# Kernel tuning notes

Hardware: AMD Instinct MI355X
Metric: run time of the kernel (lower is better)

Reference implementation:

```python
import jax, jax.numpy as jnp
import numpy as np

N = 50000      # nodes
E = 500000     # edges
IN = 128       # input feature dim
HID = 64       # hidden per-head dim
CLS = 64       # num classes
SLOPE = 0.2    # leaky_relu negative slope


def _gat_layer(x, W, al, ar, src, dst):
    """One GATConv: project, per-edge score, edge-softmax over dst, weighted aggregate.
    x: [N, Din], W: [Din, H*F], al/ar: [H, F]. Returns [N, H, F]."""
    H, F = al.shape
    n = x.shape[0]
    feat = (x @ W).reshape(n, H, F)                      # [N,H,F]
    el = jnp.einsum('nhf,hf->nh', feat, al)              # [N,H]
    er = jnp.einsum('nhf,hf->nh', feat, ar)              # [N,H]
    e = el[src] + er[dst]                                # u_add_v -> [E,H]
    e = jnp.where(e >= 0, e, SLOPE * e)                  # leaky_relu
    # edge_softmax over destination nodes (numerically stable)
    m = jax.lax.stop_gradient(jax.ops.segment_max(e, dst, num_segments=n))
    ex = jnp.exp(e - m[dst])
    denom = jax.ops.segment_sum(ex, dst, num_segments=n)
    a = ex / denom[dst]                                  # [E,H]
    # u_mul_e + sum aggregation
    out = jax.ops.segment_sum(feat[src] * a[:, :, None], dst, num_segments=n)
    return out                                           # [N,H,F]


def setup_inputs() -> dict:
    key = jax.random.key(0)
    ks = jax.random.split(key, 12)
    s = 0.05  # xavier-ish scale
    x = jax.random.normal(ks[0], (N, IN), jnp.float32)
    src = jax.random.randint(ks[1], (E,), 0, N)
    dst = jax.random.randint(ks[2], (E,), 0, N)
    W1 = jax.random.normal(ks[3], (IN, 4 * HID), jnp.float32) * s
    al1 = jax.random.normal(ks[4], (4, HID), jnp.float32) * s
    ar1 = jax.random.normal(ks[5], (4, HID), jnp.float32) * s
    W2 = jax.random.normal(ks[6], (4 * HID, 4 * HID), jnp.float32) * s
    al2 = jax.random.normal(ks[7], (4, HID), jnp.float32) * s
    ar2 = jax.random.normal(ks[8], (4, HID), jnp.float32) * s
    W3 = jax.random.normal(ks[9], (4 * HID, CLS), jnp.float32) * s
    al3 = jax.random.normal(ks[10], (1, CLS), jnp.float32) * s
    ar3 = jax.random.normal(ks[11], (1, CLS), jnp.float32) * s
    res_W3 = jax.random.normal(jax.random.fold_in(key, 99), (4 * HID, CLS), jnp.float32) * s
    return {"x": x, "W1": W1, "al1": al1, "ar1": ar1, "W2": W2, "al2": al2,
            "ar2": ar2, "W3": W3, "al3": al3, "ar3": ar3, "res_W3": res_W3,
            "src": src, "dst": dst}


def reference(x, W1, al1, ar1, W2, al2, ar2, W3, al3, ar3, res_W3, src, dst):
    # layer 0: no residual, elu activation, flatten heads
    h = _gat_layer(x, W1, al1, ar1, src, dst)            # [N,4,64]
    h = jax.nn.elu(h).reshape(N, -1)                     # [N,256]
    # layer 1: residual is Identity (in_dst 256 == 4*64), elu, flatten
    h1 = _gat_layer(h, W2, al2, ar2, src, dst)           # [N,4,64]
    h1 = h1 + h.reshape(N, 4, HID)                       # residual (Identity)
    h = jax.nn.elu(h1).reshape(N, -1)                    # [N,256]
    # layer 2: residual Linear 256->64, no activation, mean over heads
    h2 = _gat_layer(h, W3, al3, ar3, src, dst)           # [N,1,64]
    h2 = h2 + (h @ res_W3).reshape(N, 1, CLS)            # residual fc
    logits = h2.mean(axis=1)                             # [N,64]
    return logits
```

## Files before the change

### kernel.cpp

```cpp
#include <hip/hip_runtime.h>
#include <hip/hip_bf16.h>
#include <math.h>

#define SLOPE 0.2f

typedef __attribute__((ext_vector_type(8))) short short8;
typedef __attribute__((ext_vector_type(4))) float f32x4;
typedef __attribute__((ext_vector_type(4))) int   i32x4;

static __device__ __forceinline__ float leakyf(float x) { return x >= 0.f ? x : SLOPE * x; }
static __device__ __forceinline__ float bflo(unsigned u) { return __builtin_bit_cast(float, u << 16); }
static __device__ __forceinline__ float bfhi(unsigned u) { return __builtin_bit_cast(float, u & 0xffff0000u); }
static __device__ __forceinline__ unsigned short f2bf(float f) {
    unsigned u = __builtin_bit_cast(unsigned, f);
    return (unsigned short)((u + 0x7fff + ((u >> 16) & 1)) >> 16);
}

struct __align__(8) us4 { unsigned short a, b, c, d; };


__global__ __launch_bounds__(256) void tconv_all(const float* __restrict__ W1,
                                                 const float* __restrict__ W2,
                                                 const float* __restrict__ W3,
                                                 const float* __restrict__ rW3,
                                                 unsigned short* __restrict__ W1t,
                                                 unsigned short* __restrict__ W2t,
                                                 unsigned short* __restrict__ W3c) {
    int i = blockIdx.x * 256 + threadIdx.x;
    const float* W; unsigned short* Wt; int K, lNc, idx; bool permK;
    if (i < 32768)       { W = W1;  Wt = W1t;            K = 128; lNc = 8; idx = i;          permK = false; }
    else if (i < 98304)  { W = W2;  Wt = W2t;            K = 256; lNc = 8; idx = i - 32768;  permK = true; }
    else if (i < 114688) { W = W3;  Wt = W3c;            K = 256; lNc = 6; idx = i - 98304;  permK = true; }
    else                 { W = rW3; Wt = W3c + 64 * 256; K = 256; lNc = 6; idx = i - 114688; permK = true; }
    int k = idx >> lNc, n = idx & ((1 << lNc) - 1);
    int kp = permK ? ((k & ~63) | (((k & 15) << 2) | ((k & 63) >> 4))) : k;
    Wt[n * K + kp] = f2bf(W[idx]);
}

template<bool A_F32>
__global__ __launch_bounds__(256) void gemm_l12(const void* __restrict__ Av,
                                                const unsigned short* __restrict__ Wt,
                                                unsigned short* __restrict__ outb,
                                                const float* __restrict__ al,
                                                const float* __restrict__ ar,
                                                float* __restrict__ el,
                                                float* __restrict__ er,
                                                int M, int K) {
    const int lane = threadIdx.x & 63;
    const int wid = threadIdx.x >> 6;
    const int rlo = lane & 15;
    const int q = lane >> 4;
    const int kg = q * 8;
    const int m0 = blockIdx.x * 64;
    const int cbase = wid * 64;

    f32x4 acc[4][4];
#pragma unroll
    for (int mf = 0; mf < 4; ++mf)
#pragma unroll
        for (int nf = 0; nf < 4; ++nf) acc[mf][nf] = (f32x4){0.f, 0.f, 0.f, 0.f};

    for (int k0 = 0; k0 < K; k0 += 32) {
        short8 a[4];
#pragma unroll
        for (int mf = 0; mf < 4; ++mf) {
            int r = m0 + mf * 16 + rlo;
            if (r >= M) r = M - 1;
            if (A_F32) {
                const float* ap = (const float*)Av + (size_t)r * K + k0 + kg;
                float4 f0 = *(const float4*)ap;
                float4 f1 = *(const float4*)(ap + 4);
                short8 t;
                t[0] = f2bf(f0.x); t[1] = f2bf(f0.y); t[2] = f2bf(f0.z); t[3] = f2bf(f0.w);
                t[4] = f2bf(f1.x); t[5] = f2bf(f1.y); t[6] = f2bf(f1.z); t[7] = f2bf(f1.w);
                a[mf] = t;
            } else {
                a[mf] = *(const short8*)((const unsigned short*)Av + (size_t)r * K + k0 + kg);
            }
        }
#pragma unroll
        for (int nf = 0; nf < 4; ++nf) {
            short8 b = *(const short8*)(Wt + (size_t)(cbase + nf * 16 + rlo) * K + k0 + kg);
#pragma unroll
            for (int mf = 0; mf < 4; ++mf)
                acc[mf][nf] = __builtin_amdgcn_mfma_f32_16x16x32_bf16(a[mf], b, acc[mf][nf], 0, 0, 0);
        }
    }

    float alv[4], arv[4];
#pragma unroll
    for (int nf = 0; nf < 4; ++nf) {
        alv[nf] = al[cbase + nf * 16 + rlo];
        arv[nf] = ar[cbase + nf * 16 + rlo];
    }

#pragma unroll
    for (int mf = 0; mf < 4; ++mf) {
#pragma unroll
        for (int reg = 0; reg < 4; ++reg) {
            int r = m0 + mf * 16 + q * 4 + reg;
            float pl = 0.f, pr = 0.f;
#pragma unroll
            for (int nf = 0; nf < 4; ++nf) {
                pl += acc[mf][nf][reg] * alv[nf];
                pr += acc[mf][nf][reg] * arv[nf];
            }
#pragma unroll
            for (int off = 1; off < 16; off <<= 1) {
                pl += __shfl_xor(pl, off);
                pr += __shfl_xor(pr, off);
            }
            if (rlo == 0 && r < M) {
                el[(size_t)r * 4 + wid] = pl;
                er[(size_t)r * 4 + wid] = pr;
            }
            if (r < M) {
                us4 o = {f2bf(acc[mf][0][reg]), f2bf(acc[mf][1][reg]),
                         f2bf(acc[mf][2][reg]), f2bf(acc[mf][3][reg])};
                *(us4*)(outb + (size_t)r * 256 + cbase + rlo * 4) = o;
            }
        }
    }
}

__global__ __launch_bounds__(256) void gemm_l3(const unsigned short* __restrict__ A,
                                               const unsigned short* __restrict__ Wt,
                                               unsigned short* __restrict__ featb,
                                               float* __restrict__ resf,
                                               const float* __restrict__ al,
                                               const float* __restrict__ ar,
                                               float* __restrict__ el,
                                               float* __restrict__ er, int M) {
    const int K = 256;
    const int lane = threadIdx.x & 63;
    const int wid = threadIdx.x >> 6;
    const int rlo = lane & 15;
    const int q = lane >> 4;
    const int kg = q * 8;
    const int m0 = blockIdx.x * 128 + (wid >> 1) * 64;
    const int ch = wid & 1;
    const int cbase = ch * 64;

    f32x4 acc[4][4];
#pragma unroll
    for (int mf = 0; mf < 4; ++mf)
#pragma unroll
        for (int nf = 0; nf < 4; ++nf) acc[mf][nf] = (f32x4){0.f, 0.f, 0.f, 0.f};

    for (int k0 = 0; k0 < K; k0 += 32) {
        short8 a[4];
#pragma unroll
        for (int mf = 0; mf < 4; ++mf) {
            int r = m0 + mf * 16 + rlo;
            if (r >= M) r = M - 1;
            a[mf] = *(const short8*)(A + (size_t)r * K + k0 + kg);
        }
#pragma unroll
        for (int nf = 0; nf < 4; ++nf) {
            short8 b = *(const short8*)(Wt + (size_t)(cbase + nf * 16 + rlo) * K + k0 + kg);
#pragma unroll
            for (int mf = 0; mf < 4; ++mf)
                acc[mf][nf] = __builtin_amdgcn_mfma_f32_16x16x32_bf16(a[mf], b, acc[mf][nf], 0, 0, 0);
        }
    }

    float alv[4], arv[4];
    if (ch == 0) {
#pragma unroll
        for (int nf = 0; nf < 4; ++nf) {
            alv[nf] = al[nf * 16 + rlo];
            arv[nf] = ar[nf * 16 + rlo];
        }
    }

#pragma unroll
    for (int mf = 0; mf < 4; ++mf) {
#pragma unroll
        for (int reg = 0; reg < 4; ++reg) {
            int r = m0 + mf * 16 + q * 4 + reg;
            if (ch == 0) {
                float pl = 0.f, pr = 0.f;
#pragma unroll
                for (int nf = 0; nf < 4; ++nf) {
                    pl += acc[mf][nf][reg] * alv[nf];
                    pr += acc[mf][nf][reg] * arv[nf];
                }
#pragma unroll
                for (int off = 1; off < 16; off <<= 1) {
                    pl += __shfl_xor(pl, off);
                    pr += __shfl_xor(pr, off);
                }
                if (rlo == 0 && r < M) { el[r] = pl; er[r] = pr; }
                if (r < M) {
                    us4 o = {f2bf(acc[mf][0][reg]), f2bf(acc[mf][1][reg]),
                             f2bf(acc[mf][2][reg]), f2bf(acc[mf][3][reg])};
                    *(us4*)(featb + (size_t)r * 64 + rlo * 4) = o;
                }
            } else if (r < M) {
                float4 o = {acc[mf][0][reg], acc[mf][1][reg], acc[mf][2][reg], acc[mf][3][reg]};
                *(float4*)(resf + (size_t)r * 64 + rlo * 4) = o;
            }
        }
    }
}

__global__ void hist_kernel(const int* __restrict__ dst, int* __restrict__ counts, int e) {
    int i = blockIdx.x * blockDim.x + threadIdx.x;
    if (i < e) atomicAdd(&counts[dst[i]], 1);
}

__global__ __launch_bounds__(1024) void scan_block(const int* __restrict__ counts,
                                                   int* __restrict__ offsets,
                                                   int* __restrict__ bsums, int n) {
    __shared__ int ws[16];
    int tid = threadIdx.x, lane = tid & 63, wid = tid >> 6;
    int idx = blockIdx.x * 1024 + tid;
    int v = (idx < n) ? counts[idx] : 0;
    int s = v;
#pragma unroll
    for (int off = 1; off < 64; off <<= 1) {
        int t = __shfl_up(s, off);
        if (lane >= off) s += t;
    }
    if (lane == 63) ws[wid] = s;
    __syncthreads();
    if (tid < 16) {
        int w2 = ws[tid];
#pragma unroll
        for (int off = 1; off < 16; off <<= 1) {
            int t = __shfl_up(w2, off);
            if (tid >= off) w2 += t;
        }
        ws[tid] = w2;
    }
    __syncthreads();
    int wpre = wid ? ws[wid - 1] : 0;
    if (idx < n) offsets[idx] = wpre + s - v;
    if (tid == 0) bsums[blockIdx.x] = ws[15];
}

__global__ __launch_bounds__(1024) void add_off(const int* __restrict__ bsums,
                                                int* __restrict__ offsets,
                                                int* __restrict__ cursor, int n, int e, int nb) {
    __shared__ int base_s;
    int tid = threadIdx.x;
    if (tid < 64) {
        int v = (tid < blockIdx.x && tid < nb) ? bsums[tid] : 0;
#pragma unroll
        for (int off = 32; off > 0; off >>= 1) v += __shfl_xor(v, off);
        if (tid == 0) base_s = v;
    }
    __syncthreads();
    int idx = blockIdx.x * 1024 + tid;
    if (idx < n) {
        int v = offsets[idx] + base_s;
        offsets[idx] = v;
        cursor[idx] = v;
    }
    if (idx == 0) offsets[n] = e;
}

__global__ void scatter_kernel(const int* __restrict__ src, const int* __restrict__ dst,
                               int* __restrict__ cursor, int* __restrict__ csr_src,
                               int* __restrict__ csr_dst, int e) {
    int i = blockIdx.x * blockDim.x + threadIdx.x;
    if (i < e) {
        int d = dst[i];
        int pos = atomicAdd(&cursor[d], 1);
        csr_src[pos] = src[i];
        csr_dst[pos] = d;
    }
}

template<int H>
__global__ __launch_bounds__(256) void edge_scores(const int* __restrict__ csr_src,
                                                   const int* __restrict__ csr_dst,
                                                   const float* __restrict__ el,
                                                   const float* __restrict__ er,
                                                   float* __restrict__ w, int E) {
    int e4 = (blockIdx.x * 256 + threadIdx.x) * 4;
    if (e4 >= E) return;
    i32x4 s = *(const i32x4*)(csr_src + e4);
    i32x4 d = *(const i32x4*)(csr_dst + e4);
    if (H == 4) {
        float4 o0, o1, o2, o3;
        float* op[4] = {&o0.x, &o1.x, &o2.x, &o3.x};
#pragma unroll
        for (int j = 0; j < 4; ++j) {
            float4 l = *(const float4*)(el + (size_t)s[j] * 4);
            float4 r = *(const float4*)(er + (size_t)d[j] * 4);
            op[0][j] = __expf(fminf(leakyf(l.x + r.x), 80.f));
            op[1][j] = __expf(fminf(leakyf(l.y + r.y), 80.f));
            op[2][j] = __expf(fminf(leakyf(l.z + r.z), 80.f));
            op[3][j] = __expf(fminf(leakyf(l.w + r.w), 80.f));
        }
        *(float4*)(w + 0 * (size_t)E + e4) = o0;
        *(float4*)(w + 1 * (size_t)E + e4) = o1;
        *(float4*)(w + 2 * (size_t)E + e4) = o2;
        *(float4*)(w + 3 * (size_t)E + e4) = o3;
    } else {
        float4 o;
#pragma unroll
        for (int j = 0; j < 4; ++j)
            (&o.x)[j] = __expf(fminf(leakyf(el[s[j]] + er[d[j]]), 80.f));
        *(float4*)(w + e4) = o;
    }
}

template<int RES, int ACT>
__global__ __launch_bounds__(256) void gat_agg4(const unsigned short* __restrict__ fp,
                                                const float* __restrict__ wbuf,
                                                const int* __restrict__ offsets,
                                                const int* __restrict__ csr_src,
                                                const unsigned short* __restrict__ resid,
                                                unsigned short* __restrict__ outb,
                                                int n, int E) {
    int wv = threadIdx.x >> 6;
    int lane = threadIdx.x & 63;
    int half = lane >> 5;
    int sub = lane & 31;
    int node = blockIdx.x * 8 + wv * 2 + half;

    int e0 = 0, e1 = 0;
    if (node < n) { e0 = offsets[node]; e1 = offsets[node + 1]; }
    int cnt = e1 - e0;
    int ocnt = __shfl_xor(cnt, 32);
    int mc = cnt > ocnt ? cnt : ocnt;

    const float* wb = wbuf + (size_t)(sub >> 3) * E;

    float den = 0.f;
    float acc[8] = {0.f, 0.f, 0.f, 0.f, 0.f, 0.f, 0.f, 0.f};

    for (int t = 0; t < mc; t += 8) {
        i32x4 sv0, sv1;
        f32x4 wv0, wv1;
        __builtin_memcpy(&sv0, csr_src + e0 + t, 16);
        __builtin_memcpy(&sv1, csr_src + e0 + t + 4, 16);
        __builtin_memcpy(&wv0, wb + e0 + t, 16);
        __builtin_memcpy(&wv1, wb + e0 + t + 4, 16);
        int s[8];
        float w[8];
#pragma unroll
        for (int j = 0; j < 8; ++j) {
            bool ok = (t + j) < cnt;
            int sj = (j < 4) ? sv0[j] : sv1[j - 4];
            float wj = (j < 4) ? wv0[j] : wv1[j - 4];
            s[j] = ok ? sj : 0;
            w[j] = ok ? wj : 0.f;
        }
        uint4 u[8];
#pragma unroll
        for (int j = 0; j < 8; ++j)
            u[j] = *(const uint4*)(fp + (size_t)s[j] * 256 + sub * 8);
#pragma unroll
        for (int j = 0; j < 8; ++j) {
            den += w[j];
            acc[0] += w[j] * bflo(u[j].x);
            acc[1] += w[j] * bfhi(u[j].x);
            acc[2] += w[j] * bflo(u[j].y);
            acc[3] += w[j] * bfhi(u[j].y);
            acc[4] += w[j] * bflo(u[j].z);
            acc[5] += w[j] * bfhi(u[j].z);
            acc[6] += w[j] * bflo(u[j].w);
            acc[7] += w[j] * bfhi(u[j].w);
        }
    }

    if (node >= n) return;

    float inv = den > 0.f ? 1.f / den : 0.f;
    float v[8];
#pragma unroll
    for (int i = 0; i < 8; ++i) v[i] = acc[i] * inv;

    if (RES == 1) {
        uint4 ru = *(const uint4*)(resid + (size_t)node * 256 + sub * 8);
        v[0] += bflo(ru.x); v[1] += bfhi(ru.x);
        v[2] += bflo(ru.y); v[3] += bfhi(ru.y);
        v[4] += bflo(ru.z); v[5] += bfhi(ru.z);
        v[6] += bflo(ru.w); v[7] += bfhi(ru.w);
    }
    if (ACT == 1) {
#pragma unroll
        for (int i = 0; i < 8; ++i) v[i] = v[i] > 0.f ? v[i] : __expf(v[i]) - 1.f;
    }
    uint4 o;
    o.x = (unsigned)f2bf(v[0]) | ((unsigned)f2bf(v[1]) << 16);
    o.y = (unsigned)f2bf(v[2]) | ((unsigned)f2bf(v[3]) << 16);
    o.z = (unsigned)f2bf(v[4]) | ((unsigned)f2bf(v[5]) << 16);
    o.w = (unsigned)f2bf(v[6]) | ((unsigned)f2bf(v[7]) << 16);
    *(uint4*)(outb + (size_t)node * 256 + sub * 8) = o;
}

__global__ __launch_bounds__(256) void gat_agg1(const unsigned short* __restrict__ fp,
                                                const float* __restrict__ wbuf,
                                                const int* __restrict__ offsets,
                                                const int* __restrict__ csr_src,
                                                const float* __restrict__ resf,
                                                float* __restrict__ outv, int n, int E) {
    int wv = threadIdx.x >> 6;
    int lane = threadIdx.x & 63;
    int sub = lane & 15;
    int node = blockIdx.x * 16 + wv * 4 + (lane >> 4);

    int e0 = 0, e1 = 0;
    if (node < n) { e0 = offsets[node]; e1 = offsets[node + 1]; }
    int cnt = e1 - e0;
    int m1 = __shfl_xor(cnt, 16);
    int mc = cnt > m1 ? cnt : m1;
    int m2 = __shfl_xor(mc, 32);
    mc = mc > m2 ? mc : m2;

    float den = 0.f;
    float acc[4] = {0.f, 0.f, 0.f, 0.f};

    for (int t = 0; t < mc; t += 8) {
        i32x4 sv0, sv1;
        f32x4 wv0, wv1;
        __builtin_memcpy(&sv0, csr_src + e0 + t, 16);
        __builtin_memcpy(&sv1, csr_src + e0 + t + 4, 16);
        __builtin_memcpy(&wv0, wbuf + e0 + t, 16);
        __builtin_memcpy(&wv1, wbuf + e0 + t + 4, 16);
        int s[8];
        float w[8];
#pragma unroll
        for (int j = 0; j < 8; ++j) {
            bool ok = (t + j) < cnt;
            int sj = (j < 4) ? sv0[j] : sv1[j - 4];
            float wj = (j < 4) ? wv0[j] : wv1[j - 4];
            s[j] = ok ? sj : 0;
            w[j] = ok ? wj : 0.f;
        }
        uint2 u[8];
#pragma unroll
        for (int j = 0; j < 8; ++j)
            u[j] = *(const uint2*)(fp + (size_t)s[j] * 64 + sub * 4);
#pragma unroll
        for (int j = 0; j < 8; ++j) {
            den += w[j];
            acc[0] += w[j] * bflo(u[j].x);
            acc[1] += w[j] * bfhi(u[j].x);
            acc[2] += w[j] * bflo(u[j].y);
            acc[3] += w[j] * bfhi(u[j].y);
        }
    }

    if (node >= n) return;

    float inv = den > 0.f ? 1.f / den : 0.f;
    float4 rv = *(const float4*)(resf + (size_t)node * 64 + sub * 4);
    float v[4];
    v[0] = acc[0] * inv + rv.x;
    v[1] = acc[1] * inv + rv.y;
    v[2] = acc[2] * inv + rv.z;
    v[3] = acc[3] * inv + rv.w;

#pragma unroll
    for (int i = 0; i < 4; ++i) {
        int p = sub * 4 + i;
        int c = (p & 3) * 16 + (p >> 2);
        outv[(size_t)node * 64 + c] = v[i];
    }
}

extern "C" void kernel_launch(void* const* d_in, const int* in_sizes, int n_in,
                              void* d_out, int out_size, void* d_ws, size_t ws_size,
                              hipStream_t stream) {
    const float* x      = (const float*)d_in[0];
    const float* W1     = (const float*)d_in[1];
    const float* al1    = (const float*)d_in[2];
    const float* ar1    = (const float*)d_in[3];
    const float* W2     = (const float*)d_in[4];
    const float* al2    = (const float*)d_in[5];
    const float* ar2    = (const float*)d_in[6];
    const float* W3     = (const float*)d_in[7];
    const float* al3    = (const float*)d_in[8];
    const float* ar3    = (const float*)d_in[9];
    const float* res_W3 = (const float*)d_in[10];
    const int*   src    = (const int*)d_in[11];
    const int*   dst    = (const int*)d_in[12];

    const int N = in_sizes[0] / 128;
    const int E = in_sizes[11];

    float* out = (float*)d_out;

    unsigned short* featb = (unsigned short*)d_ws;
    unsigned short* h1    = featb + (size_t)N * 256;
    unsigned short* h2    = h1 + (size_t)N * 256;
    unsigned short* W1t   = h2 + (size_t)N * 256;
    unsigned short* W2t   = W1t + 256 * 128;
    unsigned short* W3c   = W2t + 256 * 256;
    float* resf = (float*)(W3c + 128 * 256);
    float* el   = resf + (size_t)N * 64;
    float* er   = el + (size_t)N * 4;
    float* wbuf = er + (size_t)N * 4;
    int* offsets = (int*)(wbuf + (size_t)E * 4);
    int* cursor  = offsets + (N + 8);
    int* csr_src = cursor + N;
    int* csr_dst = csr_src + E;
    int* bsums   = csr_dst + E;

    const int T = 256;
    const int scan_blocks = (N + 1023) / 1024;
    const int edge_blocks = (E + T - 1) / T;
    const int es_blocks = (E / 4 + T - 1) / T;

    tconv_all<<<512, T, 0, stream>>>(W1, W2, W3, res_W3, W1t, W2t, W3c);

    hipMemsetAsync(cursor, 0, (size_t)N * sizeof(int), stream);
    hist_kernel<<<edge_blocks, T, 0, stream>>>(dst, cursor, E);
    scan_block<<<scan_blocks, 1024, 0, stream>>>(cursor, offsets, bsums, N);
    add_off<<<scan_blocks, 1024, 0, stream>>>(bsums, offsets, cursor, N, E, scan_blocks);
    scatter_kernel<<<edge_blocks, T, 0, stream>>>(src, dst, cursor, csr_src, csr_dst, E);

    int gemm12_blocks = (N + 63) / 64;
    int gemm3_blocks = (N + 127) / 128;
    int agg4_blocks = (N + 7) / 8;
    int agg1_blocks = (N + 15) / 16;

    gemm_l12<true><<<gemm12_blocks, T, 0, stream>>>(x, W1t, featb, al1, ar1, el, er, N, 128);
    edge_scores<4><<<es_blocks, T, 0, stream>>>(csr_src, csr_dst, el, er, wbuf, E);
    gat_agg4<0, 1><<<agg4_blocks, T, 0, stream>>>(featb, wbuf, offsets, csr_src, nullptr, h1, N, E);

    gemm_l12<false><<<gemm12_blocks, T, 0, stream>>>(h1, W2t, featb, al2, ar2, el, er, N, 256);
    edge_scores<4><<<es_blocks, T, 0, stream>>>(csr_src, csr_dst, el, er, wbuf, E);
    gat_agg4<1, 1><<<agg4_blocks, T, 0, stream>>>(featb, wbuf, offsets, csr_src, h1, h2, N, E);

    gemm_l3<<<gemm3_blocks, T, 0, stream>>>(h2, W3c, featb, resf, al3, ar3, el, er, N);
    edge_scores<1><<<es_blocks, T, 0, stream>>>(csr_src, csr_dst, el, er, wbuf, E);
    gat_agg1<<<agg1_blocks, T, 0, stream>>>(featb, wbuf, offsets, csr_src, resf, out, N, E);
}
```

Baseline: 286.7 us.

## Fuse edge-score computation into aggregation kernels and drop the edge weight buffer

Removes the three edge_scores kernels and the per-edge weight buffer. Each aggregation thread now reads el of the source and er of the destination and computes the exp-leaky score inline. The csr_dst array and its writes are dropped, and the cursor memset is folded into the weight-conversion prep kernel. This cuts launches and the write-then-read of E*H floats, at the cost of redundant exp and el gathers per feature lane. Also pads bsums past csr_src for safe over-reads.

```diff
diff --git a/kernel.cpp b/kernel.cpp
--- a/kernel.cpp
+++ b/kernel.cpp
@@ -19,22 +19,29 @@
 struct __align__(8) us4 { unsigned short a, b, c, d; };
 
 
-__global__ __launch_bounds__(256) void tconv_all(const float* __restrict__ W1,
-                                                 const float* __restrict__ W2,
-                                                 const float* __restrict__ W3,
-                                                 const float* __restrict__ rW3,
-                                                 unsigned short* __restrict__ W1t,
-                                                 unsigned short* __restrict__ W2t,
-                                                 unsigned short* __restrict__ W3c) {
-    int i = blockIdx.x * 256 + threadIdx.x;
-    const float* W; unsigned short* Wt; int K, lNc, idx; bool permK;
-    if (i < 32768)       { W = W1;  Wt = W1t;            K = 128; lNc = 8; idx = i;          permK = false; }
-    else if (i < 98304)  { W = W2;  Wt = W2t;            K = 256; lNc = 8; idx = i - 32768;  permK = true; }
-    else if (i < 114688) { W = W3;  Wt = W3c;            K = 256; lNc = 6; idx = i - 98304;  permK = true; }
-    else                 { W = rW3; Wt = W3c + 64 * 256; K = 256; lNc = 6; idx = i - 114688; permK = true; }
-    int k = idx >> lNc, n = idx & ((1 << lNc) - 1);
-    int kp = permK ? ((k & ~63) | (((k & 15) << 2) | ((k & 63) >> 4))) : k;
-    Wt[n * K + kp] = f2bf(W[idx]);
+__global__ __launch_bounds__(256) void prep(const float* __restrict__ W1,
+                                            const float* __restrict__ W2,
+                                            const float* __restrict__ W3,
+                                            const float* __restrict__ rW3,
+                                            unsigned short* __restrict__ W1t,
+                                            unsigned short* __restrict__ W2t,
+                                            unsigned short* __restrict__ W3c,
+                                            int* __restrict__ counts, int n) {
+    int b = blockIdx.x;
+    if (b < 512) {
+        int i = b * 256 + threadIdx.x;
+        const float* W; unsigned short* Wt; int K, lNc, idx; bool permK;
+        if (i < 32768)       { W = W1;  Wt = W1t;            K = 128; lNc = 8; idx = i;          permK = false; }
+        else if (i < 98304)  { W = W2;  Wt = W2t;            K = 256; lNc = 8; idx = i - 32768;  permK = true; }
+        else if (i < 114688) { W = W3;  Wt = W3c;            K = 256; lNc = 6; idx = i - 98304;  permK = true; }
+        else                 { W = rW3; Wt = W3c + 64 * 256; K = 256; lNc = 6; idx = i - 114688; permK = true; }
+        int k = idx >> lNc, nn = idx & ((1 << lNc) - 1);
+        int kp = permK ? ((k & ~63) | (((k & 15) << 2) | ((k & 63) >> 4))) : k;
+        Wt[nn * K + kp] = f2bf(W[idx]);
+    } else {
+        int idx = (b - 512) * 256 + threadIdx.x;
+        if (idx < n) counts[idx] = 0;
+    }
 }
 
 template<bool A_F32>
@@ -261,60 +268,22 @@
 }
 
 __global__ void scatter_kernel(const int* __restrict__ src, const int* __restrict__ dst,
-                               int* __restrict__ cursor, int* __restrict__ csr_src,
-                               int* __restrict__ csr_dst, int e) {
+                               int* __restrict__ cursor, int* __restrict__ csr_src, int e) {
     int i = blockIdx.x * blockDim.x + threadIdx.x;
     if (i < e) {
-        int d = dst[i];
-        int pos = atomicAdd(&cursor[d], 1);
+        int pos = atomicAdd(&cursor[dst[i]], 1);
         csr_src[pos] = src[i];
-        csr_dst[pos] = d;
-    }
-}
-
-template<int H>
-__global__ __launch_bounds__(256) void edge_scores(const int* __restrict__ csr_src,
-                                                   const int* __restrict__ csr_dst,
-                                                   const float* __restrict__ el,
-                                                   const float* __restrict__ er,
-                                                   float* __restrict__ w, int E) {
-    int e4 = (blockIdx.x * 256 + threadIdx.x) * 4;
-    if (e4 >= E) return;
-    i32x4 s = *(const i32x4*)(csr_src + e4);
-    i32x4 d = *(const i32x4*)(csr_dst + e4);
-    if (H == 4) {
-        float4 o0, o1, o2, o3;
-        float* op[4] = {&o0.x, &o1.x, &o2.x, &o3.x};
-#pragma unroll
-        for (int j = 0; j < 4; ++j) {
-            float4 l = *(const float4*)(el + (size_t)s[j] * 4);
-            float4 r = *(const float4*)(er + (size_t)d[j] * 4);
-            op[0][j] = __expf(fminf(leakyf(l.x + r.x), 80.f));
-            op[1][j] = __expf(fminf(leakyf(l.y + r.y), 80.f));
-            op[2][j] = __expf(fminf(leakyf(l.z + r.z), 80.f));
-            op[3][j] = __expf(fminf(leakyf(l.w + r.w), 80.f));
-        }
-        *(float4*)(w + 0 * (size_t)E + e4) = o0;
-        *(float4*)(w + 1 * (size_t)E + e4) = o1;
-        *(float4*)(w + 2 * (size_t)E + e4) = o2;
-        *(float4*)(w + 3 * (size_t)E + e4) = o3;
-    } else {
-        float4 o;
-#pragma unroll
-        for (int j = 0; j < 4; ++j)
-            (&o.x)[j] = __expf(fminf(leakyf(el[s[j]] + er[d[j]]), 80.f));
-        *(float4*)(w + e4) = o;
     }
 }
 
 template<int RES, int ACT>
 __global__ __launch_bounds__(256) void gat_agg4(const unsigned short* __restrict__ fp,
-                                                const float* __restrict__ wbuf,
+                                                const float* __restrict__ el,
+                                                const float* __restrict__ er,
                                                 const int* __restrict__ offsets,
                                                 const int* __restrict__ csr_src,
                                                 const unsigned short* __restrict__ resid,
-                                                unsigned short* __restrict__ outb,
-                                                int n, int E) {
+                                                unsigned short* __restrict__ outb, int n) {
     int wv = threadIdx.x >> 6;
     int lane = threadIdx.x & 63;
     int half = lane >> 5;
@@ -327,32 +296,34 @@
     int ocnt = __shfl_xor(cnt, 32);
     int mc = cnt > ocnt ? cnt : ocnt;
 
-    const float* wb = wbuf + (size_t)(sub >> 3) * E;
+    const int hd = sub >> 3;
+    float erh = (node < n) ? er[(size_t)node * 4 + hd] : 0.f;
 
     float den = 0.f;
     float acc[8] = {0.f, 0.f, 0.f, 0.f, 0.f, 0.f, 0.f, 0.f};
 
     for (int t = 0; t < mc; t += 8) {
         i32x4 sv0, sv1;
-        f32x4 wv0, wv1;
         __builtin_memcpy(&sv0, csr_src + e0 + t, 16);
         __builtin_memcpy(&sv1, csr_src + e0 + t + 4, 16);
-        __builtin_memcpy(&wv0, wb + e0 + t, 16);
-        __builtin_memcpy(&wv1, wb + e0 + t + 4, 16);
         int s[8];
-        float w[8];
+        float msk[8];
 #pragma unroll
         for (int j = 0; j < 8; ++j) {
             bool ok = (t + j) < cnt;
-            int sj = (j < 4) ? sv0[j] : sv1[j - 4];
-            float wj = (j < 4) ? wv0[j] : wv1[j - 4];
-            s[j] = ok ? sj : 0;
-            w[j] = ok ? wj : 0.f;
+            s[j] = ok ? ((j < 4) ? sv0[j] : sv1[j - 4]) : 0;
+            msk[j] = ok ? 1.f : 0.f;
         }
         uint4 u[8];
 #pragma unroll
         for (int j = 0; j < 8; ++j)
             u[j] = *(const uint4*)(fp + (size_t)s[j] * 256 + sub * 8);
+        float w[8];
+#pragma unroll
+        for (int j = 0; j < 8; ++j) {
+            float xx = fminf(leakyf(el[(size_t)s[j] * 4 + hd] + erh), 80.f);
+            w[j] = msk[j] * __expf(xx);
+        }
 #pragma unroll
         for (int j = 0; j < 8; ++j) {
             den += w[j];
@@ -394,11 +365,12 @@
 }
 
 __global__ __launch_bounds__(256) void gat_agg1(const unsigned short* __restrict__ fp,
-                                                const float* __restrict__ wbuf,
+                                                const float* __restrict__ el,
+                                                const float* __restrict__ er,
                                                 const int* __restrict__ offsets,
                                                 const int* __restrict__ csr_src,
                                                 const float* __restrict__ resf,
-                                                float* __restrict__ outv, int n, int E) {
+                                                float* __restrict__ outv, int n) {
     int wv = threadIdx.x >> 6;
     int lane = threadIdx.x & 63;
     int sub = lane & 15;
@@ -412,30 +384,33 @@
     int m2 = __shfl_xor(mc, 32);
     mc = mc > m2 ? mc : m2;
 
+    float ern = (node < n) ? er[node] : 0.f;
+
     float den = 0.f;
     float acc[4] = {0.f, 0.f, 0.f, 0.f};
 
     for (int t = 0; t < mc; t += 8) {
         i32x4 sv0, sv1;
-        f32x4 wv0, wv1;
         __builtin_memcpy(&sv0, csr_src + e0 + t, 16);
         __builtin_memcpy(&sv1, csr_src + e0 + t + 4, 16);
-        __builtin_memcpy(&wv0, wbuf + e0 + t, 16);
-        __builtin_memcpy(&wv1, wbuf + e0 + t + 4, 16);
         int s[8];
-        float w[8];
+        float msk[8];
 #pragma unroll
         for (int j = 0; j < 8; ++j) {
             bool ok = (t + j) < cnt;
-            int sj = (j < 4) ? sv0[j] : sv1[j - 4];
-            float wj = (j < 4) ? wv0[j] : wv1[j - 4];
-            s[j] = ok ? sj : 0;
-            w[j] = ok ? wj : 0.f;
+            s[j] = ok ? ((j < 4) ? sv0[j] : sv1[j - 4]) : 0;
+            msk[j] = ok ? 1.f : 0.f;
         }
         uint2 u[8];
 #pragma unroll
         for (int j = 0; j < 8; ++j)
             u[j] = *(const uint2*)(fp + (size_t)s[j] * 64 + sub * 4);
+        float w[8];
+#pragma unroll
+        for (int j = 0; j < 8; ++j) {
+            float xx = fminf(leakyf(el[s[j]] + ern), 80.f);
+            w[j] = msk[j] * __expf(xx);
+        }
 #pragma unroll
         for (int j = 0; j < 8; ++j) {
             den += w[j];
@@ -495,25 +470,22 @@
     float* resf = (float*)(W3c + 128 * 256);
     float* el   = resf + (size_t)N * 64;
     float* er   = el + (size_t)N * 4;
-    float* wbuf = er + (size_t)N * 4;
-    int* offsets = (int*)(wbuf + (size_t)E * 4);
+    int* offsets = (int*)(er + (size_t)N * 4);
     int* cursor  = offsets + (N + 8);
     int* csr_src = cursor + N;
-    int* csr_dst = csr_src + E;
-    int* bsums   = csr_dst + E;
+    int* bsums   = csr_src + E + 256;
 
     const int T = 256;
     const int scan_blocks = (N + 1023) / 1024;
     const int edge_blocks = (E + T - 1) / T;
-    const int es_blocks = (E / 4 + T - 1) / T;
-
-    tconv_all<<<512, T, 0, stream>>>(W1, W2, W3, res_W3, W1t, W2t, W3c);
-
-    hipMemsetAsync(cursor, 0, (size_t)N * sizeof(int), stream);
+    const int zero_blocks = (N + 255) / 256;
+
+    prep<<<512 + zero_blocks, T, 0, stream>>>(W1, W2, W3, res_W3, W1t, W2t, W3c, cursor, N);
+
     hist_kernel<<<edge_blocks, T, 0, stream>>>(dst, cursor, E);
     scan_block<<<scan_blocks, 1024, 0, stream>>>(cursor, offsets, bsums, N);
     add_off<<<scan_blocks, 1024, 0, stream>>>(bsums, offsets, cursor, N, E, scan_blocks);
-    scatter_kernel<<<edge_blocks, T, 0, stream>>>(src, dst, cursor, csr_src, csr_dst, E);
+    scatter_kernel<<<edge_blocks, T, 0, stream>>>(src, dst, cursor, csr_src, E);
 
     int gemm12_blocks = (N + 63) / 64;
     int gemm3_blocks = (N + 127) / 128;
@@ -521,14 +493,11 @@
     int agg1_blocks = (N + 15) / 16;
 
     gemm_l12<true><<<gemm12_blocks, T, 0, stream>>>(x, W1t, featb, al1, ar1, el, er, N, 128);
-    edge_scores<4><<<es_blocks, T, 0, stream>>>(csr_src, csr_dst, el, er, wbuf, E);
-    gat_agg4<0, 1><<<agg4_blocks, T, 0, stream>>>(featb, wbuf, offsets, csr_src, nullptr, h1, N, E);
+    gat_agg4<0, 1><<<agg4_blocks, T, 0, stream>>>(featb, el, er, offsets, csr_src, nullptr, h1, N);
 
     gemm_l12<false><<<gemm12_blocks, T, 0, stream>>>(h1, W2t, featb, al2, ar2, el, er, N, 256);
-    edge_scores<4><<<es_blocks, T, 0, stream>>>(csr_src, csr_dst, el, er, wbuf, E);
-    gat_agg4<1, 1><<<agg4_blocks, T, 0, stream>>>(featb, wbuf, offsets, csr_src, h1, h2, N, E);
+    gat_agg4<1, 1><<<agg4_blocks, T, 0, stream>>>(featb, el, er, offsets, csr_src, h1, h2, N);
 
     gemm_l3<<<gemm3_blocks, T, 0, stream>>>(h2, W3c, featb, resf, al3, ar3, el, er, N);
-    edge_scores<1><<<es_blocks, T, 0, stream>>>(csr_src, csr_dst, el, er, wbuf, E);
-    gat_agg1<<<agg1_blocks, T, 0, stream>>>(featb, wbuf, offsets, csr_src, resf, out, N, E);
-}
+    gat_agg1<<<agg1_blocks, T, 0, stream>>>(featb, el, er, offsets, csr_src, resf, out, N);
+}
```

Measured after the change: 292.3 us. No clear change (+1.9%).

## Fuse preprocessing launches: merge memset into prep, lookback scan, co-launch scatter with GEMM1

Applied to the files above, without the earlier changes.

Folds the weight conversion and the zeroing of the counts array into one prep kernel. It replaces the two-pass block scan with a single-pass decoupled lookback scan that uses flags, and runs the CSR scatter in the same grid as the layer-1 GEMM as extra blocks. The aim is to remove several small kernel launches and serialization bubbles at the start of the pipeline. The lookback scan spins on flags set by earlier blocks, so it depends on lower-numbered blocks being scheduled first. With only 49 blocks that is safe in practice.

```diff
diff --git a/kernel.cpp b/kernel.cpp
--- a/kernel.cpp
+++ b/kernel.cpp
@@ -19,39 +19,48 @@
 struct __align__(8) us4 { unsigned short a, b, c, d; };
 
 
-__global__ __launch_bounds__(256) void tconv_all(const float* __restrict__ W1,
-                                                 const float* __restrict__ W2,
-                                                 const float* __restrict__ W3,
-                                                 const float* __restrict__ rW3,
-                                                 unsigned short* __restrict__ W1t,
-                                                 unsigned short* __restrict__ W2t,
-                                                 unsigned short* __restrict__ W3c) {
-    int i = blockIdx.x * 256 + threadIdx.x;
-    const float* W; unsigned short* Wt; int K, lNc, idx; bool permK;
-    if (i < 32768)       { W = W1;  Wt = W1t;            K = 128; lNc = 8; idx = i;          permK = false; }
-    else if (i < 98304)  { W = W2;  Wt = W2t;            K = 256; lNc = 8; idx = i - 32768;  permK = true; }
-    else if (i < 114688) { W = W3;  Wt = W3c;            K = 256; lNc = 6; idx = i - 98304;  permK = true; }
-    else                 { W = rW3; Wt = W3c + 64 * 256; K = 256; lNc = 6; idx = i - 114688; permK = true; }
-    int k = idx >> lNc, n = idx & ((1 << lNc) - 1);
-    int kp = permK ? ((k & ~63) | (((k & 15) << 2) | ((k & 63) >> 4))) : k;
-    Wt[n * K + kp] = f2bf(W[idx]);
+__global__ __launch_bounds__(256) void prep(const float* __restrict__ W1,
+                                            const float* __restrict__ W2,
+                                            const float* __restrict__ W3,
+                                            const float* __restrict__ rW3,
+                                            unsigned short* __restrict__ W1t,
+                                            unsigned short* __restrict__ W2t,
+                                            unsigned short* __restrict__ W3c,
+                                            int* __restrict__ counts,
+                                            int* __restrict__ bflag, int n) {
+    int b = blockIdx.x;
+    if (b < 512) {
+        int i = b * 256 + threadIdx.x;
+        const float* W; unsigned short* Wt; int K, lNc, idx; bool permK;
+        if (i < 32768)       { W = W1;  Wt = W1t;            K = 128; lNc = 8; idx = i;          permK = false; }
+        else if (i < 98304)  { W = W2;  Wt = W2t;            K = 256; lNc = 8; idx = i - 32768;  permK = true; }
+        else if (i < 114688) { W = W3;  Wt = W3c;            K = 256; lNc = 6; idx = i - 98304;  permK = true; }
+        else                 { W = rW3; Wt = W3c + 64 * 256; K = 256; lNc = 6; idx = i - 114688; permK = true; }
+        int k = idx >> lNc, nn = idx & ((1 << lNc) - 1);
+        int kp = permK ? ((k & ~63) | (((k & 15) << 2) | ((k & 63) >> 4))) : k;
+        Wt[nn * K + kp] = f2bf(W[idx]);
+    } else {
+        if (b == 512 && threadIdx.x < 64) bflag[threadIdx.x] = 0;
+        int idx = (b - 512) * 256 + threadIdx.x;
+        if (idx < n) counts[idx] = 0;
+    }
 }
 
 template<bool A_F32>
-__global__ __launch_bounds__(256) void gemm_l12(const void* __restrict__ Av,
-                                                const unsigned short* __restrict__ Wt,
-                                                unsigned short* __restrict__ outb,
-                                                const float* __restrict__ al,
-                                                const float* __restrict__ ar,
-                                                float* __restrict__ el,
-                                                float* __restrict__ er,
-                                                int M, int K) {
+static __device__ __forceinline__ void gemm_l12_body(int bid, const void* __restrict__ Av,
+                                                     const unsigned short* __restrict__ Wt,
+                                                     unsigned short* __restrict__ outb,
+                                                     const float* __restrict__ al,
+                                                     const float* __restrict__ ar,
+                                                     float* __restrict__ el,
+                                                     float* __restrict__ er,
+                                                     int M, int K) {
     const int lane = threadIdx.x & 63;
     const int wid = threadIdx.x >> 6;
     const int rlo = lane & 15;
     const int q = lane >> 4;
     const int kg = q * 8;
-    const int m0 = blockIdx.x * 64;
+    const int m0 = bid * 64;
     const int cbase = wid * 64;
 
     f32x4 acc[4][4];
@@ -119,6 +128,44 @@
                          f2bf(acc[mf][2][reg]), f2bf(acc[mf][3][reg])};
                 *(us4*)(outb + (size_t)r * 256 + cbase + rlo * 4) = o;
             }
+        }
+    }
+}
+
+template<bool A_F32>
+__global__ __launch_bounds__(256) void gemm_l12(const void* __restrict__ Av,
+                                                const unsigned short* __restrict__ Wt,
+                                                unsigned short* __restrict__ outb,
+                                                const float* __restrict__ al,
+                                                const float* __restrict__ ar,
+                                                float* __restrict__ el,
+                                                float* __restrict__ er, int M, int K) {
+    gemm_l12_body<A_F32>(blockIdx.x, Av, Wt, outb, al, ar, el, er, M, K);
+}
+
+__global__ __launch_bounds__(256) void gemm1_scatter(const float* __restrict__ x,
+                                                     const unsigned short* __restrict__ W1t,
+                                                     unsigned short* __restrict__ featb,
+                                                     const float* __restrict__ al,
+                                                     const float* __restrict__ ar,
+                                                     float* __restrict__ el,
+                                                     float* __restrict__ er,
+                                                     int M, int K, int gemm_blocks,
+                                                     const int* __restrict__ src,
+                                                     const int* __restrict__ dst,
+                                                     int* __restrict__ cursor,
+                                                     int* __restrict__ csr_src,
+                                                     int* __restrict__ csr_dst, int E) {
+    int b = blockIdx.x;
+    if (b < gemm_blocks) {
+        gemm_l12_body<true>(b, x, W1t, featb, al, ar, el, er, M, K);
+    } else {
+        int i = (b - gemm_blocks) * 256 + threadIdx.x;
+        if (i < E) {
+            int d = dst[i];
+            int pos = atomicAdd(&cursor[d], 1);
+            csr_src[pos] = src[i];
+            csr_dst[pos] = d;
         }
     }
 }
@@ -209,12 +256,15 @@
     if (i < e) atomicAdd(&counts[dst[i]], 1);
 }
 
-__global__ __launch_bounds__(1024) void scan_block(const int* __restrict__ counts,
-                                                   int* __restrict__ offsets,
-                                                   int* __restrict__ bsums, int n) {
+__global__ __launch_bounds__(1024) void scan_lookback(const int* __restrict__ counts,
+                                                      int* __restrict__ offsets,
+                                                      int* __restrict__ cursor,
+                                                      int* __restrict__ bsum,
+                                                      int* __restrict__ bflag, int n, int e) {
     __shared__ int ws[16];
-    int tid = threadIdx.x, lane = tid & 63, wid = tid >> 6;
-    int idx = blockIdx.x * 1024 + tid;
+    __shared__ int base_s;
+    int tid = threadIdx.x, lane = tid & 63, wid = tid >> 6, bid = blockIdx.x;
+    int idx = bid * 1024 + tid;
     int v = (idx < n) ? counts[idx] : 0;
     int s = v;
 #pragma unroll
@@ -234,42 +284,28 @@
         ws[tid] = w2;
     }
     __syncthreads();
-    int wpre = wid ? ws[wid - 1] : 0;
-    if (idx < n) offsets[idx] = wpre + s - v;
-    if (tid == 0) bsums[blockIdx.x] = ws[15];
-}
-
-__global__ __launch_bounds__(1024) void add_off(const int* __restrict__ bsums,
-                                                int* __restrict__ offsets,
-                                                int* __restrict__ cursor, int n, int e, int nb) {
-    __shared__ int base_s;
-    int tid = threadIdx.x;
-    if (tid < 64) {
-        int v = (tid < blockIdx.x && tid < nb) ? bsums[tid] : 0;
-#pragma unroll
-        for (int off = 32; off > 0; off >>= 1) v += __shfl_xor(v, off);
-        if (tid == 0) base_s = v;
+    int local_ex = (wid ? ws[wid - 1] : 0) + s - v;
+    if (tid == 0) {
+        __hip_atomic_store(&bsum[bid], ws[15], __ATOMIC_RELAXED, __HIP_MEMORY_SCOPE_AGENT);
+        __hip_atomic_store(&bflag[bid], 1, __ATOMIC_RELEASE, __HIP_MEMORY_SCOPE_AGENT);
+    }
+    if (wid == 0) {
+        int acc = 0;
+        for (int p = lane; p < bid; p += 64) {
+            while (__hip_atomic_load(&bflag[p], __ATOMIC_ACQUIRE, __HIP_MEMORY_SCOPE_AGENT) == 0) {}
+            acc += __hip_atomic_load(&bsum[p], __ATOMIC_RELAXED, __HIP_MEMORY_SCOPE_AGENT);
+        }
+#pragma unroll
+        for (int off = 32; off > 0; off >>= 1) acc += __shfl_xor(acc, off);
+        if (lane == 0) base_s = acc;
     }
     __syncthreads();
-    int idx = blockIdx.x * 1024 + tid;
+    int val = base_s + local_ex;
     if (idx < n) {
-        int v = offsets[idx] + base_s;
-        offsets[idx] = v;
-        cursor[idx] = v;
+        offsets[idx] = val;
+        cursor[idx] = val;
     }
     if (idx == 0) offsets[n] = e;
-}
-
-__global__ void scatter_kernel(const int* __restrict__ src, const int* __restrict__ dst,
-                               int* __restrict__ cursor, int* __restrict__ csr_src,
-                               int* __restrict__ csr_dst, int e) {
-    int i = blockIdx.x * blockDim.x + threadIdx.x;
-    if (i < e) {
-        int d = dst[i];
-        int pos = atomicAdd(&cursor[d], 1);
-        csr_src[pos] = src[i];
-        csr_dst[pos] = d;
-    }
 }
 
 template<int H>
@@ -499,35 +535,32 @@
     int* offsets = (int*)(wbuf + (size_t)E * 4);
     int* cursor  = offsets + (N + 8);
     int* csr_src = cursor + N;
-    int* csr_dst = csr_src + E;
+    int* csr_dst = csr_src + E + 64;
     int* bsums   = csr_dst + E;
+    int* bflag   = bsums + 64;
 
     const int T = 256;
     const int scan_blocks = (N + 1023) / 1024;
     const int edge_blocks = (E + T - 1) / T;
+    const int zero_blocks = (N + 255) / 256;
     const int es_blocks = (E / 4 + T - 1) / T;
-
-    tconv_all<<<512, T, 0, stream>>>(W1, W2, W3, res_W3, W1t, W2t, W3c);
-
-    hipMemsetAsync(cursor, 0, (size_t)N * sizeof(int), stream);
-    hist_kernel<<<edge_blocks, T, 0, stream>>>(dst, cursor, E);
-    scan_block<<<scan_blocks, 1024, 0, stream>>>(cursor, offsets, bsums, N);
-    add_off<<<scan_blocks, 1024, 0, stream>>>(bsums, offsets, cursor, N, E, scan_blocks);
-    scatter_kernel<<<edge_blocks, T, 0, stream>>>(src, dst, cursor, csr_src, csr_dst, E);
 
     int gemm12_blocks = (N + 63) / 64;
     int gemm3_blocks = (N + 127) / 128;
     int agg4_blocks = (N + 7) / 8;
     int agg1_blocks = (N + 15) / 16;
 
-    gemm_l12<true><<<gemm12_blocks, T, 0, stream>>>(x, W1t, featb, al1, ar1, el, er, N, 128);
+    prep<<<512 + zero_blocks, T, 0, stream>>>(W1, W2, W3, res_W3, W1t, W2t, W3c, cursor, bflag, N);
+    hist_kernel<<<edge_blocks, T, 0, stream>>>(dst, cursor, E);
+    scan_lookback<<<scan_blocks, 1024, 0, stream>>>(cursor, offsets, cursor, bsums, bflag, N, E);
+    gemm1_scatter<<<gemm12_blocks + edge_blocks, T, 0, stream>>>(x, W1t, featb, al1, ar1, el, er,
+                                                                 N, 128, gemm12_blocks,
+                                                                 src, dst, cursor, csr_src, csr_dst, E);
     edge_scores<4><<<es_blocks, T, 0, stream>>>(csr_src, csr_dst, el, er, wbuf, E);
     gat_agg4<0, 1><<<agg4_blocks, T, 0, stream>>>(featb, wbuf, offsets, csr_src, nullptr, h1, N, E);
-
     gemm_l12<false><<<gemm12_blocks, T, 0, stream>>>(h1, W2t, featb, al2, ar2, el, er, N, 256);
     edge_scores<4><<<es_blocks, T, 0, stream>>>(csr_src, csr_dst, el, er, wbuf, E);
     gat_agg4<1, 1><<<agg4_blocks, T, 0, stream>>>(featb, wbuf, offsets, csr_src, h1, h2, N, E);
-
     gemm_l3<<<gemm3_blocks, T, 0, stream>>>(h2, W3c, featb, resf, al3, ar3, el, er, N);
     edge_scores<1><<<es_blocks, T, 0, stream>>>(csr_src, csr_dst, el, er, wbuf, E);
     gat_agg1<<<agg1_blocks, T, 0, stream>>>(featb, wbuf, offsets, csr_src, resf, out, N, E);
```

New measurement: 273.9 us. 1.05x faster.
